# Optimization experiments

Measured on AMD Instinct MI355X. Metric: run time of the kernel, lower is better.

Reference implementation:

```python
import jax, jax.numpy as jnp
import numpy as np
import math

K_L = 16
EPS = 1e-5


def _knn_idx(xyt, k):
    # xyt: [B,N,3] -> idx of k nearest (incl. self), ascending distance. [B,N,k]
    sq = jnp.sum(xyt * xyt, axis=-1)                      # [B,N]
    d2 = sq[:, :, None] + sq[:, None, :] - 2.0 * jnp.einsum('bnd,bmd->bnm', xyt, xyt)
    _, idx = jax.lax.top_k(-d2, k)                        # smallest distances first
    return idx


def _gather(x, idx):
    # x: [B,N,D], idx: [B,N,K] -> [B,N,K,D]
    return jax.vmap(lambda p, i: p[i])(x, idx)


def setup_inputs() -> dict:
    key = jax.random.key(0)
    ks = jax.random.split(key, 6)
    B, N, C_in, C = 4, 8192, 64, 64
    xytp = jax.random.normal(ks[0], (B, N, 4), jnp.float32)
    features = jax.random.normal(ks[1], (B, N, C_in), jnp.float32)
    pe_w1 = jax.random.normal(ks[2], (4, C), jnp.float32) * (1.0 / math.sqrt(4))
    pe_b1 = jnp.zeros((C,), jnp.float32)
    pe_w2 = jax.random.normal(ks[3], (C, C), jnp.float32) * (1.0 / math.sqrt(C))
    pe_b2 = jnp.zeros((C,), jnp.float32)
    lt_w = jax.random.normal(ks[4], (C_in, 3 * C), jnp.float32) * (1.0 / math.sqrt(C_in))
    lt_b = jnp.zeros((3 * C,), jnp.float32)
    ln_g = jnp.ones((C,), jnp.float32)
    ln_b = jnp.zeros((C,), jnp.float32)
    return dict(xytp=xytp, features=features, pe_w1=pe_w1, pe_b1=pe_b1,
                pe_w2=pe_w2, pe_b2=pe_b2, lt_w=lt_w, lt_b=lt_b,
                ln_g=ln_g, ln_b=ln_b)


def reference(xytp, features, pe_w1, pe_b1, pe_w2, pe_b2, lt_w, lt_b, ln_g, ln_b):
    C = ln_g.shape[0]
    scale = math.sqrt(C)
    xyt = jax.lax.stop_gradient(xytp[:, :, :3])
    idx = _knn_idx(xyt, K_L)                              # [B,N,K]

    # relative position encoding: MLP(Linear-ReLU-Linear) on xytp deltas
    rel = xytp[:, :, None, :] - _gather(xytp, idx)        # [B,N,K,4]
    delta = jax.nn.relu(rel @ pe_w1 + pe_b1) @ pe_w2 + pe_b2  # [B,N,K,C]

    lt = features @ lt_w + lt_b                           # [B,N,3C]
    varphi, psi, alpha = lt[..., :C], lt[..., C:2 * C], lt[..., 2 * C:]
    psi_g = _gather(psi, idx)                             # [B,N,K,C]
    alpha_g = _gather(alpha, idx)                         # [B,N,K,C]

    pre = varphi[:, :, None, :] - psi_g + delta           # [B,N,K,C]
    mu = jnp.mean(pre, axis=-1, keepdims=True)
    var = jnp.mean((pre - mu) ** 2, axis=-1, keepdims=True)
    ln = (pre - mu) * jax.lax.rsqrt(var + EPS) * ln_g + ln_b

    attn = jax.nn.softmax(ln / scale, axis=2)             # softmax over K
    return jnp.sum(attn * (alpha_g + delta), axis=2)      # [B,N,C]
```

## Files before the change

kernel.cpp:

```cpp
#include <hip/hip_runtime.h>
#include <stdint.h>

#define BATCH 4
#define NPTS 8192
#define KNN_K 16
#define GRID 24
#define NCELL (GRID * GRID * GRID)
#define NCELLP (NCELL + 8)

typedef unsigned long long u64;
typedef unsigned int u32;
typedef unsigned short u16;

#define WS_IDX 0u
#define WS_LT 1048576u
#define WS_CNT 26214400u
#define WS_OFF 26435584u
#define WS_CUR 26656896u
#define WS_SP 26878080u
#define WS_GP 27402368u
#define WS_SIDX 27402496u

#define NQBLK ((BATCH * NPTS) / 8)
#define NLBLK ((BATCH * NPTS) / 32)

__device__ __forceinline__ int cellof(float v, float o, float invs) {
  int c = (int)((v - o) * invs);
  return c < GRID - 1 ? c : GRID - 1;
}

__device__ __forceinline__ u32 f2bf(float v) {
  u32 x = __float_as_uint(v);
  return (x + 0x7FFFu + ((x >> 16) & 1u)) >> 16;
}

typedef _Float16 hv2 __attribute__((ext_vector_type(2)));
union U32H2 { u32 u; hv2 h; };
__device__ __forceinline__ float fdot2u(u32 a, u32 b, float c) {
  U32H2 x, y; x.u = a; y.u = b;
  return __builtin_amdgcn_fdot2(x.h, y.h, c, false);
}
__device__ __forceinline__ u16 f16b(float v) {
  union { _Float16 f; u16 b; } c; c.f = (_Float16)v; return c.b;
}
__device__ __forceinline__ u32 pkf16(float a, float b) {
  return (u32)f16b(a) | ((u32)f16b(b) << 16);
}

__global__ __launch_bounds__(256) void k_bbox1(const float4* __restrict__ xytp,
                                               float* __restrict__ part,
                                               int* __restrict__ cnt) {
  const int blk = blockIdx.x;
  const int b = blk >> 5, sub = blk & 31;
  const int t = threadIdx.x;
#pragma unroll
  for (int i = 0; i < 2; ++i) {
    int v = t + i * 256;
    if (v < 432) cnt[blk * 432 + v] = 0;
  }
  float4 p = xytp[(b << 13) + (sub << 8) + t];
  float mnx = p.x, mny = p.y, mnz = p.z;
  float mxx = p.x, mxy = p.y, mxz = p.z;
#pragma unroll
  for (int d = 1; d < 64; d <<= 1) {
    mnx = fminf(mnx, __shfl_xor(mnx, d)); mny = fminf(mny, __shfl_xor(mny, d));
    mnz = fminf(mnz, __shfl_xor(mnz, d)); mxx = fmaxf(mxx, __shfl_xor(mxx, d));
    mxy = fmaxf(mxy, __shfl_xor(mxy, d)); mxz = fmaxf(mxz, __shfl_xor(mxz, d));
  }
  __shared__ float red[4][6];
  const int lane = t & 63, wv = t >> 6;
  if (lane == 0) {
    red[wv][0] = mnx; red[wv][1] = mny; red[wv][2] = mnz;
    red[wv][3] = mxx; red[wv][4] = mxy; red[wv][5] = mxz;
  }
  __syncthreads();
  if (t == 0) {
    for (int w = 1; w < 4; ++w) {
      red[0][0] = fminf(red[0][0], red[w][0]);
      red[0][1] = fminf(red[0][1], red[w][1]);
      red[0][2] = fminf(red[0][2], red[w][2]);
      red[0][3] = fmaxf(red[0][3], red[w][3]);
      red[0][4] = fmaxf(red[0][4], red[w][4]);
      red[0][5] = fmaxf(red[0][5], red[w][5]);
    }
    float* o = part + blk * 8;
    o[0] = red[0][0]; o[1] = red[0][1]; o[2] = red[0][2];
    o[3] = red[0][3]; o[4] = red[0][4]; o[5] = red[0][5];
  }
}

__global__ __launch_bounds__(64) void k_bbox2(const float* __restrict__ part,
                                              float* __restrict__ gp) {
  const int b = blockIdx.x, t = threadIdx.x;
  const float* pp = part + (b * 32 + (t & 31)) * 8;
  float mnx = pp[0], mny = pp[1], mnz = pp[2];
  float mxx = pp[3], mxy = pp[4], mxz = pp[5];
#pragma unroll
  for (int d = 1; d < 64; d <<= 1) {
    mnx = fminf(mnx, __shfl_xor(mnx, d)); mny = fminf(mny, __shfl_xor(mny, d));
    mnz = fminf(mnz, __shfl_xor(mnz, d)); mxx = fmaxf(mxx, __shfl_xor(mxx, d));
    mxy = fmaxf(mxy, __shfl_xor(mxy, d)); mxz = fmaxf(mxz, __shfl_xor(mxz, d));
  }
  if (t == 0) {
    float rmax = fmaxf(mxx - mnx, fmaxf(mxy - mny, mxz - mnz));
    float s = rmax / (float)GRID;
    float* g = gp + b * 8;
    g[0] = mnx; g[1] = mny; g[2] = mnz;
    g[3] = s; g[4] = 1.0f / s;
  }
}

__global__ __launch_bounds__(256) void k_count(const float4* __restrict__ xytp,
                                               const float* __restrict__ gp,
                                               int* __restrict__ cnt) {
  int i = blockIdx.x * 256 + threadIdx.x;
  int b = i >> 13;
  const float* g = gp + b * 8;
  float4 p = xytp[i];
  int cx = cellof(p.x, g[0], g[4]);
  int cy = cellof(p.y, g[1], g[4]);
  int cz = cellof(p.z, g[2], g[4]);
  atomicAdd(&cnt[b * NCELL + (cz * GRID + cy) * GRID + cx], 1);
}

__global__ __launch_bounds__(1024) void k_scan(const int* __restrict__ cnt,
                                               int* __restrict__ offs,
                                               int* __restrict__ curs) {
  __shared__ int wsum[16];
  const int b = blockIdx.x, t = threadIdx.x;
  const int base = b * NCELL;
  const int base2 = b * NCELLP;
  const int lo = t * 14;
  const int hi = lo + 14 < NCELL ? lo + 14 : NCELL;
  int s = 0;
  for (int c = lo; c < hi; ++c) s += cnt[base + c];
  const int lane = t & 63, wv = t >> 6;
  int v = s;
#pragma unroll
  for (int d = 1; d < 64; d <<= 1) {
    int u = __shfl_up(v, d);
    if (lane >= d) v += u;
  }
  if (lane == 63) wsum[wv] = v;
  __syncthreads();
  if (wv == 0 && lane < 16) {
    int x = wsum[lane];
#pragma unroll
    for (int d = 1; d < 16; d <<= 1) {
      int u = __shfl_up(x, d, 16);
      if (lane >= d) x += u;
    }
    wsum[lane] = x;
  }
  __syncthreads();
  int excl = (wv > 0 ? wsum[wv - 1] : 0) + v - s;
  for (int c = lo; c < hi; ++c) {
    offs[base2 + c] = excl;
    curs[base + c] = excl;
    excl += cnt[base + c];
  }
  if (hi == NCELL) offs[base2 + NCELL] = excl;
}

__global__ __launch_bounds__(256) void k_scatter(const float4* __restrict__ xytp,
                                                 const float* __restrict__ gp,
                                                 int* __restrict__ curs,
                                                 float4* __restrict__ spts,
                                                 u16* __restrict__ sidx) {
  int i = blockIdx.x * 256 + threadIdx.x;
  int b = i >> 13, n = i & 8191;
  const float* g = gp + b * 8;
  float4 p = xytp[i];
  int cx = cellof(p.x, g[0], g[4]);
  int cy = cellof(p.y, g[1], g[4]);
  int cz = cellof(p.z, g[2], g[4]);
  int pos = atomicAdd(&curs[b * NCELL + (cz * GRID + cy) * GRID + cx], 1);
  float sq = fmaf(p.z, p.z, fmaf(p.y, p.y, p.x * p.x));
  spts[(b << 13) + pos] = make_float4(p.x, p.y, p.z, sq);
  sidx[(b << 13) + pos] = (u16)n;
}

__global__ __launch_bounds__(1024) void k_order(const float4* __restrict__ spts,
                                                const int* __restrict__ offs,
                                                const float* __restrict__ gp,
                                                u16* __restrict__ ord) {
  __shared__ int hist[32];
  __shared__ int strt[32];
  const int b = blockIdx.x, t = threadIdx.x;
  if (t < 32) hist[t] = 0;
  __syncthreads();
  const float* g = gp + b * 8;
  const int* ob = offs + b * NCELLP;
  const float4* sp = spts + (b << 13);
  int key[8];
#pragma unroll
  for (int it = 0; it < 8; ++it) {
    const int i = t + it * 1024;
    float4 p = sp[i];
    int cx = cellof(p.x, g[0], g[4]);
    int cy = cellof(p.y, g[1], g[4]);
    int cz = cellof(p.z, g[2], g[4]);
    int c = (cz * GRID + cy) * GRID + cx;
    int cc = ob[c + 1] - ob[c];
    key[it] = cc - 1 < 31 ? cc - 1 : 31;
    atomicAdd(&hist[key[it]], 1);
  }
  __syncthreads();
  if (t == 0) {
    int acc = 0;
    for (int k2 = 0; k2 < 32; ++k2) { strt[k2] = acc; acc += hist[k2]; }
  }
  __syncthreads();
  u16* ob2 = ord + (b << 13);
#pragma unroll
  for (int it = 0; it < 8; ++it) {
    const int i = t + it * 1024;
    int pos = atomicAdd(&strt[key[it]], 1);
    ob2[pos] = (u16)i;
  }
}

#define INSERTC(Af, OI)                                                      \
  {                                                                          \
    float dot = q.x * (Af).x;                                                \
    dot = fmaf(q.y, (Af).y, dot);                                            \
    dot = fmaf(q.z, (Af).z, dot);                                            \
    float d2 = (qsq + (Af).w) - 2.0f * dot;                                  \
    unsigned u = __float_as_uint(d2);                                        \
    u ^= (0x80000000u | (unsigned)((int)u >> 31));                           \
    u64 key = ((u64)u << 32) | (OI);                                         \
    if (key < lst[15]) {                                                     \
      u64 x = key;                                                           \
      _Pragma("unroll") for (int p = 0; p < 16; ++p) {                       \
        bool sw = x < lst[p];                                                \
        u64 a = lst[p];                                                      \
        lst[p] = sw ? x : a;                                                 \
        x = sw ? a : x;                                                      \
      }                                                                      \
    }                                                                        \
  }

#define CSWAP(ia, ib)                                                        \
  {                                                                          \
    u64 ta = c[ia], tb2 = c[ib];                                             \
    bool sw = ta > tb2;                                                      \
    c[ia] = sw ? tb2 : ta;                                                   \
    c[ib] = sw ? ta : tb2;                                                   \
  }

__global__ __launch_bounds__(256) void k_query(
    const float4* __restrict__ spts, const u16* __restrict__ sidx,
    const int* __restrict__ offs, const float* __restrict__ gp,
    const u16* __restrict__ ord, u16* __restrict__ oidx,
    const float* __restrict__ feat, const float* __restrict__ ltw,
    const float* __restrict__ ltb, float* __restrict__ lt) {
  __shared__ float sw_c[16][196];
  __shared__ float sf_c[32][18];
  const int tid = threadIdx.x;

  if (blockIdx.x >= NQBLK) {
    const int r0 = (blockIdx.x - NQBLK) * 32;
    const int r = tid >> 3;
    const int c0 = (tid & 7) * 8;
    float acc[24];
#pragma unroll
    for (int m = 0; m < 8; ++m) {
      acc[m] = ltb[c0 + m];
      acc[8 + m] = ltb[64 + c0 + m];
      acc[16 + m] = ltb[128 + c0 + m];
    }
    for (int ch = 0; ch < 4; ++ch) {
#pragma unroll
      for (int i = 0; i < 3; ++i) {
        int f = tid + i * 256;
        int row = f / 48, col4 = f % 48;
        float4 w4 = ((const float4*)ltw)[(ch * 16 + row) * 48 + col4];
        *(float4*)&sw_c[row][col4 * 4] = w4;
      }
      {
        int v = tid * 2;
        int row = v >> 4, jj = v & 15;
        const float2 f2 =
            *(const float2*)(feat + (size_t)(r0 + row) * 64 + ch * 16 + jj);
        sf_c[row][jj] = f2.x;
        sf_c[row][jj + 1] = f2.y;
      }
      __syncthreads();
#pragma unroll 4
      for (int jj = 0; jj < 16; ++jj) {
        float f = sf_c[r][jj];
#pragma unroll
        for (int sec = 0; sec < 3; ++sec) {
          float4 w4a = *(const float4*)&sw_c[jj][sec * 64 + c0];
          float4 w4b = *(const float4*)&sw_c[jj][sec * 64 + c0 + 4];
          acc[sec * 8 + 0] = fmaf(f, w4a.x, acc[sec * 8 + 0]);
          acc[sec * 8 + 1] = fmaf(f, w4a.y, acc[sec * 8 + 1]);
          acc[sec * 8 + 2] = fmaf(f, w4a.z, acc[sec * 8 + 2]);
          acc[sec * 8 + 3] = fmaf(f, w4a.w, acc[sec * 8 + 3]);
          acc[sec * 8 + 4] = fmaf(f, w4b.x, acc[sec * 8 + 4]);
          acc[sec * 8 + 5] = fmaf(f, w4b.y, acc[sec * 8 + 5]);
          acc[sec * 8 + 6] = fmaf(f, w4b.z, acc[sec * 8 + 6]);
          acc[sec * 8 + 7] = fmaf(f, w4b.w, acc[sec * 8 + 7]);
        }
      }
      __syncthreads();
    }
    float* orow = lt + (size_t)(r0 + r) * 128;
    *(float4*)&orow[c0] = make_float4(acc[0], acc[1], acc[2], acc[3]);
    *(float4*)&orow[c0 + 4] = make_float4(acc[4], acc[5], acc[6], acc[7]);
    u32 pk[8];
#pragma unroll
    for (int m = 0; m < 8; ++m)
      pk[m] = f2bf(acc[8 + m]) | (f2bf(acc[16 + m]) << 16);
    u32* prow = (u32*)orow + 64 + c0;
    *(uint4*)&prow[0] = make_uint4(pk[0], pk[1], pk[2], pk[3]);
    *(uint4*)&prow[4] = make_uint4(pk[4], pk[5], pk[6], pk[7]);
    return;
  }

  const int lane = tid & 63;
  const int l = tid & 31;
  const int qid = blockIdx.x * 8 + (tid >> 5);
  const int b = qid >> 13;
  const int i = ord[(b << 13) + (qid & 8191)];
  const int tb = lane & 32;
  const float4* __restrict__ sp = spts + (b << 13);
  const u16* __restrict__ sx = sidx + (b << 13);
  const int* __restrict__ ob = offs + b * NCELLP;
  const float* g = gp + b * 8;
  float4 q = sp[i];
  const float qsq = q.w;
  const unsigned orig = sx[i];
  const int cx = cellof(q.x, g[0], g[4]);
  const int cy = cellof(q.y, g[1], g[4]);
  const int cz = cellof(q.z, g[2], g[4]);
  const float s = g[3];
  const float fx = q.x - fmaf((float)cx, s, g[0]);
  const float fy = q.y - fmaf((float)cy, s, g[1]);
  const float fz = q.z - fmaf((float)cz, s, g[2]);
  const float mn = fmaxf(
      0.0f, fminf(fminf(fminf(fx, s - fx), fminf(fy, s - fy)),
                  fminf(fz, s - fz)));

  u64 lst[16];
#pragma unroll
  for (int p = 0; p < 16; ++p) lst[p] = ~0ULL;

  for (int r = 0; r <= GRID; ++r) {
    const int W = 2 * r + 1;
    const int nent = 2 * W * W;
    for (int cb = 0; cb < nent; cb += 32) {
      int ms0 = 0, ms1 = 0;
      const int eid = cb + l;
      if (eid < nent) {
        const int rid = eid >> 1, side = eid & 1;
        const int dz = rid / W - r;
        const int dy = rid % W - r;
        const int z2 = cz + dz, y2 = cy + dy;
        if ((unsigned)z2 < GRID && (unsigned)y2 < GRID) {
          const int rowb = (z2 * GRID + y2) * GRID;
          const bool bdry = (dz == -r) || (dz == r) || (dy == -r) || (dy == r);
          if (bdry) {
            if (side == 0) {
              const int xl = cx - r < 0 ? 0 : cx - r;
              const int xh = cx + r > GRID - 1 ? GRID - 1 : cx + r;
              ms0 = ob[rowb + xl];
              ms1 = ob[rowb + xh + 1];
            }
          } else {
            const int x2 = side ? cx + r : cx - r;
            if ((unsigned)x2 < GRID) {
              ms0 = ob[rowb + x2];
              ms1 = ob[rowb + x2 + 1];
            }
          }
        }
      }
      const int len = ms1 - ms0;
      int pre = len;
#pragma unroll
      for (int d = 1; d < 32; d <<= 1) {
        int u2 = __shfl_up(pre, d);
        if (l >= d) pre += u2;
      }
      const int total = __shfl(pre, tb + 31);
      if (total == 0) continue;
      const int base = ms0 - (pre - len);
      for (int vb = 0; vb < total; vb += 32) {
        const int vidx = vb + l;
        int e = 0;
#pragma unroll
        for (int s2 = 16; s2 >= 1; s2 >>= 1) {
          int pv = __shfl(pre, tb + e + s2 - 1);
          if (pv <= vidx) e += s2;
        }
        const int jb = __shfl(base, tb + e);
        if (vidx < total) {
          const int j = jb + vidx;
          float4 A = sp[j];
          unsigned oi = sx[j];
          INSERTC(A, oi)
        }
      }
    }
    const float rs = fmaf((float)r, s, mn);
    const float T = fmaf(rs, rs, -1e-4f);
    unsigned tu = __float_as_uint(T);
    tu ^= (0x80000000u | (unsigned)((int)tu >> 31));
    int c = 0;
#pragma unroll
    for (int p = 0; p < 16; ++p) c += ((unsigned)(lst[p] >> 32) <= tu) ? 1 : 0;
    c += __shfl_xor(c, 1);
    c += __shfl_xor(c, 2);
    c += __shfl_xor(c, 4);
    c += __shfl_xor(c, 8);
    c += __shfl_xor(c, 16);
    if (c >= 16) break;
  }

#pragma unroll
  for (int mm = 1; mm <= 16; mm <<= 1) {
    u64 c[16];
    const bool keepmin = (l & mm) == 0;
#pragma unroll
    for (int p = 0; p < 16; ++p) {
      u64 o = __shfl_xor(lst[15 - p], mm);
      u64 a = lst[p];
      u64 lo = a < o ? a : o;
      u64 hi = a < o ? o : a;
      c[p] = keepmin ? lo : hi;
    }
    CSWAP(0, 8) CSWAP(1, 9) CSWAP(2, 10) CSWAP(3, 11)
    CSWAP(4, 12) CSWAP(5, 13) CSWAP(6, 14) CSWAP(7, 15)
    CSWAP(0, 4) CSWAP(1, 5) CSWAP(2, 6) CSWAP(3, 7)
    CSWAP(8, 12) CSWAP(9, 13) CSWAP(10, 14) CSWAP(11, 15)
    CSWAP(0, 2) CSWAP(1, 3) CSWAP(4, 6) CSWAP(5, 7)
    CSWAP(8, 10) CSWAP(9, 11) CSWAP(12, 14) CSWAP(13, 15)
    CSWAP(0, 1) CSWAP(2, 3) CSWAP(4, 5) CSWAP(6, 7)
    CSWAP(8, 9) CSWAP(10, 11) CSWAP(12, 13) CSWAP(14, 15)
#pragma unroll
    for (int p = 0; p < 16; ++p) lst[p] = c[p];
  }

  if (l == 0) {
    unsigned pk[8];
#pragma unroll
    for (int k = 0; k < 16; k += 2)
      pk[k >> 1] = (unsigned)(lst[k] & 0xFFFFull) |
                   ((unsigned)(lst[k + 1] & 0xFFFFull) << 16);
    unsigned* od = (unsigned*)(oidx + (((size_t)(b << 13) + orig) << 4));
#pragma unroll
    for (int k = 0; k < 8; ++k) od[k] = pk[k];
  }
}

template <int CTRL>
__device__ __forceinline__ float dpp_add_f(float x) {
  int y = __builtin_amdgcn_update_dpp(0, __float_as_int(x), CTRL, 0xf, 0xf,
                                      true);
  return x + __int_as_float(y);
}
__device__ __forceinline__ float wave_sum64(float x) {
  x = dpp_add_f<0x111>(x);
  x = dpp_add_f<0x112>(x);
  x = dpp_add_f<0x114>(x);
  x = dpp_add_f<0x118>(x);
  x = dpp_add_f<0x142>(x);
  x = dpp_add_f<0x143>(x);
  return __int_as_float(__builtin_amdgcn_readlane(__float_as_int(x), 63));
}

__global__ __launch_bounds__(256) void k_main(
    const float4* __restrict__ xytp, const float* __restrict__ lt,
    const u16* __restrict__ knn, const float* __restrict__ pe_w1,
    const float* __restrict__ pe_b1, const float* __restrict__ pe_w2,
    const float* __restrict__ pe_b2, const float* __restrict__ ln_g,
    const float* __restrict__ ln_b, float* __restrict__ out) {
  __shared__ u16 s_h[4][16][64];
  const int lane = threadIdx.x & 63;
  const int wave = threadIdx.x >> 6;
  const int pid = __builtin_amdgcn_readfirstlane(blockIdx.x * 4 + wave);
  const int b = pid >> 13;
  const int n = pid & 8191;

  float w1c[4];
#pragma unroll
  for (int d = 0; d < 4; ++d) w1c[d] = pe_w1[d * 64 + lane];
  const float b1c = pe_b1[lane];
  u32 w2pk[32];
#pragma unroll
  for (int m2 = 0; m2 < 32; ++m2) {
    float a = pe_w2[(2 * m2) * 64 + lane];
    float bb = pe_w2[(2 * m2 + 1) * 64 + lane];
    w2pk[m2] = pkf16(a, bb);
  }
  const float b2c = pe_b2[lane];
  const float gc = ln_g[lane], bc = ln_b[lane];

  int nb[16];
#pragma unroll
  for (int k = 0; k < 16; ++k) nb[k] = knn[pid * 16 + k];

  const float* __restrict__ ltb = lt + (size_t)(b << 13) * 128;
  const float vc = ltb[(size_t)n * 128 + lane];

  const float4 qv = xytp[(b << 13) + n];
#pragma unroll
  for (int k = 0; k < 16; ++k) {
    float4 g = xytp[(b << 13) + nb[k]];
    float r0 = qv.x - g.x, r1 = qv.y - g.y, r2 = qv.z - g.z, r3 = qv.w - g.w;
    float h = fmaf(r3, w1c[3],
                   fmaf(r2, w1c[2], fmaf(r1, w1c[1], fmaf(r0, w1c[0], b1c))));
    s_h[wave][k][lane] = f16b(fmaxf(h, 0.0f));
  }
  __syncthreads();

  u32 uA = ((const u32*)(ltb + (size_t)nb[0] * 128 + 64))[lane];
  u32 uB = ((const u32*)(ltb + (size_t)nb[1] * 128 + 64))[lane];
  float m = -INFINITY, se = 0.f, oacc = 0.f;
#pragma unroll
  for (int k = 0; k < 16; ++k) {
    const u32 uc = (k & 1) ? uB : uA;
    if (k < 14) {
      const u32* prow = (const u32*)(ltb + (size_t)nb[k + 2] * 128 + 64);
      if (k & 1) uB = prow[lane];
      else       uA = prow[lane];
    }
    const float psi_c = __uint_as_float(uc << 16);
    const float alp_c = __uint_as_float(uc & 0xFFFF0000u);
    float acc = b2c;
    const uint4* hp = (const uint4*)&s_h[wave][k][0];
#pragma unroll
    for (int j4 = 0; j4 < 8; ++j4) {
      uint4 hv = hp[j4];
      acc = fdot2u(hv.x, w2pk[j4 * 4 + 0], acc);
      acc = fdot2u(hv.y, w2pk[j4 * 4 + 1], acc);
      acc = fdot2u(hv.z, w2pk[j4 * 4 + 2], acc);
      acc = fdot2u(hv.w, w2pk[j4 * 4 + 3], acc);
    }
    const float pre = (vc - psi_c) + acc;
    const float apd = alp_c + acc;
    const float sm = wave_sum64(pre);
    const float ssm = wave_sum64(pre * pre);
    const float mu = sm * 0.015625f;
    const float var = fmaf(ssm, 0.015625f, -mu * mu);
    const float inv = rsqrtf(var + 1e-5f);
    const float x = fmaf((pre - mu) * inv, gc, bc) * 0.125f;
    const float mn = fmaxf(m, x);
    const float corr = __expf(m - mn);
    const float e = __expf(x - mn);
    se = fmaf(se, corr, e);
    oacc = fmaf(oacc, corr, e * apd);
    m = mn;
  }
  out[(size_t)pid * 64 + lane] = oacc / se;
}

extern "C" void kernel_launch(void* const* d_in, const int* in_sizes, int n_in,
                              void* d_out, int out_size, void* d_ws,
                              size_t ws_size, hipStream_t stream) {
  const float4* xytp = (const float4*)d_in[0];
  const float* features = (const float*)d_in[1];
  const float* pe_w1 = (const float*)d_in[2];
  const float* pe_b1 = (const float*)d_in[3];
  const float* pe_w2 = (const float*)d_in[4];
  const float* pe_b2 = (const float*)d_in[5];
  const float* lt_w = (const float*)d_in[6];
  const float* lt_b = (const float*)d_in[7];
  const float* ln_g = (const float*)d_in[8];
  const float* ln_b = (const float*)d_in[9];
  float* out = (float*)d_out;

  char* ws = (char*)d_ws;
  u16* idxbuf = (u16*)(ws + WS_IDX);
  float* lt = (float*)(ws + WS_LT);
  int* cnt = (int*)(ws + WS_CNT);
  int* offs = (int*)(ws + WS_OFF);
  int* curs = (int*)(ws + WS_CUR);
  float4* spts = (float4*)(ws + WS_SP);
  float* gp = (float*)(ws + WS_GP);
  u16* sidx = (u16*)(ws + WS_SIDX);
  u16* ordb = (u16*)(ws + WS_CNT);

  k_bbox1<<<128, 256, 0, stream>>>(xytp, (float*)(ws + WS_CUR), cnt);
  k_bbox2<<<BATCH, 64, 0, stream>>>((const float*)(ws + WS_CUR), gp);
  k_count<<<(BATCH * NPTS) / 256, 256, 0, stream>>>(xytp, gp, cnt);
  k_scan<<<BATCH, 1024, 0, stream>>>(cnt, offs, curs);
  k_scatter<<<(BATCH * NPTS) / 256, 256, 0, stream>>>(xytp, gp, curs, spts,
                                                      sidx);
  k_order<<<BATCH, 1024, 0, stream>>>(spts, offs, gp, ordb);
  k_query<<<NQBLK + NLBLK, 256, 0, stream>>>(spts, sidx, offs, gp, ordb,
                                             idxbuf, features, lt_w, lt_b,
                                             lt);
  k_main<<<(BATCH * NPTS) / 4, 256, 0, stream>>>(xytp, lt, idxbuf, pe_w1,
                                                 pe_b1, pe_w2, pe_b2, ln_g,
                                                 ln_b, out);
}
```

Baseline: 336.1 us.

## Fuse bbox reduction into count and build cell-size ordering inside scan

The bbox final reduction now runs redundantly in every k_count wavefront, so the separate k_bbox2 launch goes away. The k_order kernel is removed, and its work moves into k_scan, which builds the density-sorted point order from per-cell counts it already holds in registers. Whole cells are placed in the order by atomics on cell counts, so per-point reloads of spts and offsets are no longer needed. This removes two kernel launches and a pass over sorted points. The cost is serial per-thread loops in a 4-block scan kernel, and the ord buffer moves to its own workspace region.

```diff
diff --git a/kernel.cpp b/kernel.cpp
--- a/kernel.cpp
+++ b/kernel.cpp
@@ -14,6 +14,7 @@
 
 #define WS_IDX 0u
 #define WS_LT 1048576u
+#define WS_ORD 17825792u
 #define WS_CNT 26214400u
 #define WS_OFF 26435584u
 #define WS_CUR 26656896u
@@ -89,10 +90,14 @@
   }
 }
 
-__global__ __launch_bounds__(64) void k_bbox2(const float* __restrict__ part,
-                                              float* __restrict__ gp) {
-  const int b = blockIdx.x, t = threadIdx.x;
-  const float* pp = part + (b * 32 + (t & 31)) * 8;
+__global__ __launch_bounds__(256) void k_count(const float4* __restrict__ xytp,
+                                               const float* __restrict__ part,
+                                               float* __restrict__ gp,
+                                               int* __restrict__ cnt) {
+  int i = blockIdx.x * 256 + threadIdx.x;
+  int b = i >> 13;
+  const int lane = threadIdx.x & 63;
+  const float* pp = part + (b * 32 + (lane & 31)) * 8;
   float mnx = pp[0], mny = pp[1], mnz = pp[2];
   float mxx = pp[3], mxy = pp[4], mxz = pp[5];
 #pragma unroll
@@ -101,39 +106,41 @@
     mnz = fminf(mnz, __shfl_xor(mnz, d)); mxx = fmaxf(mxx, __shfl_xor(mxx, d));
     mxy = fmaxf(mxy, __shfl_xor(mxy, d)); mxz = fmaxf(mxz, __shfl_xor(mxz, d));
   }
-  if (t == 0) {
-    float rmax = fmaxf(mxx - mnx, fmaxf(mxy - mny, mxz - mnz));
-    float s = rmax / (float)GRID;
+  float rmax = fmaxf(mxx - mnx, fmaxf(mxy - mny, mxz - mnz));
+  float s = rmax / (float)GRID;
+  float invs = 1.0f / s;
+  if ((blockIdx.x & 31) == 0 && threadIdx.x == 0) {
     float* g = gp + b * 8;
     g[0] = mnx; g[1] = mny; g[2] = mnz;
-    g[3] = s; g[4] = 1.0f / s;
-  }
-}
-
-__global__ __launch_bounds__(256) void k_count(const float4* __restrict__ xytp,
-                                               const float* __restrict__ gp,
-                                               int* __restrict__ cnt) {
-  int i = blockIdx.x * 256 + threadIdx.x;
-  int b = i >> 13;
-  const float* g = gp + b * 8;
+    g[3] = s; g[4] = invs;
+  }
   float4 p = xytp[i];
-  int cx = cellof(p.x, g[0], g[4]);
-  int cy = cellof(p.y, g[1], g[4]);
-  int cz = cellof(p.z, g[2], g[4]);
+  int cx = cellof(p.x, mnx, invs);
+  int cy = cellof(p.y, mny, invs);
+  int cz = cellof(p.z, mnz, invs);
   atomicAdd(&cnt[b * NCELL + (cz * GRID + cy) * GRID + cx], 1);
 }
 
 __global__ __launch_bounds__(1024) void k_scan(const int* __restrict__ cnt,
                                                int* __restrict__ offs,
-                                               int* __restrict__ curs) {
+                                               int* __restrict__ curs,
+                                               u16* __restrict__ ord) {
   __shared__ int wsum[16];
+  __shared__ int hist[32];
+  __shared__ int strt[32];
   const int b = blockIdx.x, t = threadIdx.x;
   const int base = b * NCELL;
   const int base2 = b * NCELLP;
   const int lo = t * 14;
   const int hi = lo + 14 < NCELL ? lo + 14 : NCELL;
+  const int nc = hi - lo;
+  int c14[14];
   int s = 0;
-  for (int c = lo; c < hi; ++c) s += cnt[base + c];
+  for (int j = 0; j < nc; ++j) {
+    c14[j] = cnt[base + lo + j];
+    s += c14[j];
+  }
+  if (t < 32) hist[t] = 0;
   const int lane = t & 63, wv = t >> 6;
   int v = s;
 #pragma unroll
@@ -153,13 +160,38 @@
     wsum[lane] = x;
   }
   __syncthreads();
-  int excl = (wv > 0 ? wsum[wv - 1] : 0) + v - s;
-  for (int c = lo; c < hi; ++c) {
-    offs[base2 + c] = excl;
-    curs[base + c] = excl;
-    excl += cnt[base + c];
+  const int excl0 = (wv > 0 ? wsum[wv - 1] : 0) + v - s;
+  int excl = excl0;
+  for (int j = 0; j < nc; ++j) {
+    offs[base2 + lo + j] = excl;
+    curs[base + lo + j] = excl;
+    excl += c14[j];
   }
   if (hi == NCELL) offs[base2 + NCELL] = excl;
+  for (int j = 0; j < nc; ++j) {
+    int cc = c14[j];
+    if (cc > 0) {
+      int key = cc - 1 < 31 ? cc - 1 : 31;
+      atomicAdd(&hist[key], cc);
+    }
+  }
+  __syncthreads();
+  if (t == 0) {
+    int acc = 0;
+    for (int k2 = 0; k2 < 32; ++k2) { strt[k2] = acc; acc += hist[k2]; }
+  }
+  __syncthreads();
+  u16* ob2 = ord + (b << 13);
+  int e = excl0;
+  for (int j = 0; j < nc; ++j) {
+    int cc = c14[j];
+    if (cc > 0) {
+      int key = cc - 1 < 31 ? cc - 1 : 31;
+      int pos = atomicAdd(&strt[key], cc);
+      for (int q2 = 0; q2 < cc; ++q2) ob2[pos + q2] = (u16)(e + q2);
+    }
+    e += cc;
+  }
 }
 
 __global__ __launch_bounds__(256) void k_scatter(const float4* __restrict__ xytp,
@@ -178,46 +210,6 @@
   float sq = fmaf(p.z, p.z, fmaf(p.y, p.y, p.x * p.x));
   spts[(b << 13) + pos] = make_float4(p.x, p.y, p.z, sq);
   sidx[(b << 13) + pos] = (u16)n;
-}
-
-__global__ __launch_bounds__(1024) void k_order(const float4* __restrict__ spts,
-                                                const int* __restrict__ offs,
-                                                const float* __restrict__ gp,
-                                                u16* __restrict__ ord) {
-  __shared__ int hist[32];
-  __shared__ int strt[32];
-  const int b = blockIdx.x, t = threadIdx.x;
-  if (t < 32) hist[t] = 0;
-  __syncthreads();
-  const float* g = gp + b * 8;
-  const int* ob = offs + b * NCELLP;
-  const float4* sp = spts + (b << 13);
-  int key[8];
-#pragma unroll
-  for (int it = 0; it < 8; ++it) {
-    const int i = t + it * 1024;
-    float4 p = sp[i];
-    int cx = cellof(p.x, g[0], g[4]);
-    int cy = cellof(p.y, g[1], g[4]);
-    int cz = cellof(p.z, g[2], g[4]);
-    int c = (cz * GRID + cy) * GRID + cx;
-    int cc = ob[c + 1] - ob[c];
-    key[it] = cc - 1 < 31 ? cc - 1 : 31;
-    atomicAdd(&hist[key[it]], 1);
-  }
-  __syncthreads();
-  if (t == 0) {
-    int acc = 0;
-    for (int k2 = 0; k2 < 32; ++k2) { strt[k2] = acc; acc += hist[k2]; }
-  }
-  __syncthreads();
-  u16* ob2 = ord + (b << 13);
-#pragma unroll
-  for (int it = 0; it < 8; ++it) {
-    const int i = t + it * 1024;
-    int pos = atomicAdd(&strt[key[it]], 1);
-    ob2[pos] = (u16)i;
-  }
 }
 
 #define INSERTC(Af, OI)                                                      \
@@ -580,15 +572,14 @@
   float4* spts = (float4*)(ws + WS_SP);
   float* gp = (float*)(ws + WS_GP);
   u16* sidx = (u16*)(ws + WS_SIDX);
-  u16* ordb = (u16*)(ws + WS_CNT);
+  u16* ordb = (u16*)(ws + WS_ORD);
 
   k_bbox1<<<128, 256, 0, stream>>>(xytp, (float*)(ws + WS_CUR), cnt);
-  k_bbox2<<<BATCH, 64, 0, stream>>>((const float*)(ws + WS_CUR), gp);
-  k_count<<<(BATCH * NPTS) / 256, 256, 0, stream>>>(xytp, gp, cnt);
-  k_scan<<<BATCH, 1024, 0, stream>>>(cnt, offs, curs);
+  k_count<<<(BATCH * NPTS) / 256, 256, 0, stream>>>(
+      xytp, (const float*)(ws + WS_CUR), gp, cnt);
+  k_scan<<<BATCH, 1024, 0, stream>>>(cnt, offs, curs, ordb);
   k_scatter<<<(BATCH * NPTS) / 256, 256, 0, stream>>>(xytp, gp, curs, spts,
                                                       sidx);
-  k_order<<<BATCH, 1024, 0, stream>>>(spts, offs, gp, ordb);
   k_query<<<NQBLK + NLBLK, 256, 0, stream>>>(spts, sidx, offs, gp, ordb,
                                              idxbuf, features, lt_w, lt_b,
                                              lt);
```

Measured after the change: 327.1 us. 2.7% less time.
